# Kernel optimization log

Hardware: AMD Instinct MI355X
Metric: run time of the kernel (lower is better)

Reference implementation:

```python
import jax, jax.numpy as jnp
import numpy as np

B, S, H, OUT, L = 32, 4096, 128, 128, 3


def _log_g(x):
    return jnp.where(x >= 0, jnp.log(jax.nn.relu(x) + 0.5), -jax.nn.softplus(-x))


def _cell(x, Wz, bz, Wh, bh):
    # x: [B, S, Din] -> h: [B, S, H]
    k = x @ Wz.T + bz                              # [B,S,H]
    log_z = -jax.nn.softplus(-k)
    log_coeffs = -jax.nn.softplus(k)
    # h_0 = zeros -> log_g(0) = log(0.5)
    log_h0 = jnp.full((x.shape[0], 1, k.shape[-1]), np.log(0.5), dtype=k.dtype)
    log_tilde_h = _log_g(x @ Wh.T + bh)
    log_values = jnp.concatenate([log_h0, log_z + log_tilde_h], axis=1)  # [B,S+1,H]
    # FAITHFUL to source: cumsum over the FEATURE axis (dim=-1), pad along seq
    a_star = jnp.pad(jnp.cumsum(log_coeffs, axis=-1), ((0, 0), (1, 0), (0, 0)))
    log_h = a_star + jax.lax.cumlogsumexp(log_values - a_star, axis=1)
    # torch forward applies sigmoid to the cell output, then drops the h_0 row
    return jax.nn.sigmoid(jnp.exp(log_h))[:, 1:, :]


def setup_inputs() -> dict:
    key = jax.random.key(0)
    ks = jax.random.split(key, 2 * L + 2)
    inp = {"x": jax.random.normal(ks[0], (B, S), dtype=jnp.float32)}
    for l in range(L):
        din = 1 if l == 0 else H
        inp[f"Wz{l}"] = jax.random.normal(ks[1 + 2 * l], (H, din), dtype=jnp.float32) * 0.02
        inp[f"bz{l}"] = jnp.zeros((H,), dtype=jnp.float32)
        inp[f"Wh{l}"] = jax.random.normal(ks[2 + 2 * l], (H, din), dtype=jnp.float32) * 0.02
        inp[f"bh{l}"] = jnp.zeros((H,), dtype=jnp.float32)
    inp["Wout"] = jax.random.normal(ks[-1], (OUT, H * S), dtype=jnp.float32) * (1.0 / np.sqrt(H * S))
    inp["bout"] = jnp.zeros((OUT,), dtype=jnp.float32)
    return inp


def reference(x, Wz0, bz0, Wh0, bh0, Wz1, bz1, Wh1, bh1, Wz2, bz2, Wh2, bh2, Wout, bout):
    h = x[:, :, None]  # [B,S,1]
    for (Wz, bz, Wh, bh) in ((Wz0, bz0, Wh0, bh0), (Wz1, bz1, Wh1, bh1), (Wz2, bz2, Wh2, bh2)):
        h = _cell(h, Wz, bz, Wh, bh)
    flat = h.reshape(h.shape[0], -1)  # [B, S*H]
    return flat @ Wout.T + bout       # [B, OUT]
```

## Files before the change

### kernel.cpp

```cpp
#include <hip/hip_runtime.h>
#include <hip/hip_bf16.h>
#include <math.h>

#define B_   32
#define S_   4096
#define H_   128
#define OUT_ 128
#define P_   (B_*S_)
#define NC_  64
#define CH_  (S_/NC_)
#define NKS_ 512
#define KTOT_ (H_*S_)
#define NEGINF_ (-__builtin_inff())
#define HTP_ 136

typedef __bf16 bf16x8 __attribute__((ext_vector_type(8)));
typedef float  f32x4  __attribute__((ext_vector_type(4)));
typedef unsigned short ushort8_t __attribute__((ext_vector_type(8)));

__device__ __forceinline__ float sp_(float x) {
  return __logf(1.f + __expf(x));
}
__device__ __forceinline__ float logg_(float x) {
  float t = (x >= 0.f) ? (x + 0.5f) : __builtin_amdgcn_rcpf(1.f + __expf(-x));
  return __logf(t);
}
__device__ __forceinline__ float lae_(float a, float b) {
  float m = fmaxf(a, b);
  float d = -fabsf(a - b);
  return m + __logf(1.f + __expf(d));
}
__device__ __forceinline__ float sigm_(float e) {
  return __builtin_amdgcn_rcpf(1.f + __expf(-e));
}
__device__ __forceinline__ unsigned short f2bf_(float f) {
  unsigned int u = __float_as_uint(f);
  u += 0x7fffu + ((u >> 16) & 1u);
  return (unsigned short)(u >> 16);
}

#define DPPADD_(v, ctrl, rmask) \
  ((v) + __int_as_float(__builtin_amdgcn_update_dpp( \
      0, __float_as_int(v), (ctrl), (rmask), 0xf, true)))
__device__ __forceinline__ float wscan_(float v) {
  v = DPPADD_(v, 0x111, 0xf);
  v = DPPADD_(v, 0x112, 0xf);
  v = DPPADD_(v, 0x114, 0xf);
  v = DPPADD_(v, 0x118, 0xf);
  v = DPPADD_(v, 0x142, 0xa);
  v = DPPADD_(v, 0x143, 0xc);
  return v;
}

__global__ __launch_bounds__(256) void convw2_kernel(
    const float* __restrict__ Wz1, const float* __restrict__ Wh1,
    const float* __restrict__ Wz2, const float* __restrict__ Wh2,
    unsigned short* __restrict__ Wc1, unsigned short* __restrict__ Wc2)
{
  int idx = blockIdx.x * 256 + threadIdx.x;
  Wc1[idx] = f2bf_(idx < 16384 ? Wz1[idx] : Wh1[idx - 16384]);
  Wc2[idx] = f2bf_(idx < 16384 ? Wz2[idx] : Wh2[idx - 16384]);
}

__global__ __launch_bounds__(256) void prep0t_kernel(
    const float* __restrict__ x,
    const float* __restrict__ Wz, const float* __restrict__ bz,
    const float* __restrict__ Wh, const float* __restrict__ bh,
    float* __restrict__ u, float* __restrict__ A, float* __restrict__ tot)
{
  __shared__ float tpart[4][128];
  int lane = threadIdx.x & 63, w = threadIdx.x >> 6;
  float wz0 = Wz[lane], wz1 = Wz[lane + 64];
  float bz0 = bz[lane], bz1 = bz[lane + 64];
  float wh0 = Wh[lane], wh1 = Wh[lane + 64];
  float bh0 = bh[lane], bh1 = bh[lane + 64];
  int blk = blockIdx.x;
  size_t base = (size_t)blk * (CH_ * H_);
  int pos0 = blk * CH_;
  float t0 = NEGINF_, t1 = NEGINF_;
  for (int j = 0; j < 16; ++j) {
    int i = j * 4 + w;
    float xv = x[pos0 + i];
    float k0 = fmaf(xv, wz0, bz0), k1 = fmaf(xv, wz1, bz1);
    float g0 = fmaf(xv, wh0, bh0), g1 = fmaf(xv, wh1, bh1);
    float lc0 = -sp_(k0), lc1 = -sp_(k1);
    float lv0 = k0 + lc0 + logg_(g0);
    float lv1 = k1 + lc1 + logg_(g1);
    float s0 = wscan_(lc0);
    float c0 = __shfl(s0, 63, 64);
    float s1 = wscan_(lc1) + c0;
    float u0 = lv0 - s0, u1 = lv1 - s1;
    size_t o = base + (size_t)i * H_;
    u[o + lane]      = u0;  u[o + 64 + lane] = u1;
    A[o + lane]      = s0;  A[o + 64 + lane] = s1;
    t0 = lae_(t0, u0); t1 = lae_(t1, u1);
  }
  tpart[w][lane] = t0; tpart[w][64 + lane] = t1;
  __syncthreads();
  if (w == 0) {
    int ch = lane;
    tot[(size_t)blk * H_ + ch] =
        lae_(lae_(tpart[0][ch], tpart[1][ch]), lae_(tpart[2][ch], tpart[3][ch]));
    ch = lane + 64;
    tot[(size_t)blk * H_ + ch] =
        lae_(lae_(tpart[0][ch], tpart[1][ch]), lae_(tpart[2][ch], tpart[3][ch]));
  }
}

__global__ __launch_bounds__(128) void scan2_kernel(
    const float* __restrict__ tot, float* __restrict__ carry)
{
  int b = blockIdx.x, ch = threadIdx.x;
  float r = -0.6931471805599453f;
  for (int c = 0; c < NC_; ++c) {
    size_t idx = (size_t)(b * NC_ + c) * H_ + ch;
    carry[idx] = r;
    r = lae_(r, tot[idx]);
  }
}

__global__ __launch_bounds__(256) void kb_kernel(
    const float* __restrict__ carry,
    const unsigned short* __restrict__ Wc,
    const float* __restrict__ bz, const float* __restrict__ bh,
    float* __restrict__ u, float* __restrict__ A,
    float* __restrict__ tot)
{
  __shared__ unsigned short hT[64][HTP_];
  __shared__ float kg[16][260];
  __shared__ float scr[32][128];
  __shared__ float thand[128];
  __shared__ float tpart[4][128];
  int tid = threadIdx.x;
  int lane = tid & 63, w = tid >> 6;
  int l15 = lane & 15, quad = lane >> 4;
  int half = tid >> 7, ch = tid & 127;
  int blk = blockIdx.x;
  size_t base = (size_t)blk * (CH_ * H_);

  if (half == 0) {
    float r = carry[(size_t)blk * H_ + ch];
    const float* up = u + base + ch;
    const float* Ap = A + base + ch;
    for (int i0 = 0; i0 < 32; i0 += 16) {
      float uv[16], av[16];
      #pragma unroll
      for (int i = 0; i < 16; ++i) { uv[i] = up[(i0 + i) * H_]; av[i] = Ap[(i0 + i) * H_]; }
      #pragma unroll
      for (int i = 0; i < 16; ++i) {
        r = lae_(r, uv[i]);
        hT[i0 + i][ch] = f2bf_(sigm_(__expf(av[i] + r)));
      }
    }
    thand[ch] = r;
  } else {
    float r = NEGINF_;
    const float* up = u + base + ch;
    for (int i0 = 0; i0 < 32; i0 += 16) {
      float uv[16];
      #pragma unroll
      for (int i = 0; i < 16; ++i) uv[i] = up[(32 + i0 + i) * H_];
      #pragma unroll
      for (int i = 0; i < 16; ++i) { r = lae_(r, uv[i]); scr[i0 + i][ch] = r; }
    }
  }
  __syncthreads();
  if (half == 1) {
    float r31 = thand[ch];
    const float* Ap = A + base + ch;
    for (int i0 = 0; i0 < 32; i0 += 16) {
      float av[16];
      #pragma unroll
      for (int i = 0; i < 16; ++i) av[i] = Ap[(32 + i0 + i) * H_];
      #pragma unroll
      for (int i = 0; i < 16; ++i) {
        float ri = lae_(r31, scr[i0 + i][ch]);
        hT[32 + i0 + i][ch] = f2bf_(sigm_(__expf(av[i] + ri)));
      }
    }
  }
  __syncthreads();

  float bz0v = bz[lane], bz1v = bz[lane + 64];
  float bh0v = bh[lane], bh1v = bh[lane + 64];
  float t0 = NEGINF_, t1 = NEGINF_;

  for (int t = 0; t < 4; ++t) {
    f32x4 z = {0.f, 0.f, 0.f, 0.f};
    f32x4 acc[4] = {z, z, z, z};
    #pragma unroll
    for (int kk = 0; kk < 4; ++kk) {
      bf16x8 a = *reinterpret_cast<const bf16x8*>(&hT[t * 16 + l15][kk * 32 + quad * 8]);
      #pragma unroll
      for (int nt = 0; nt < 4; ++nt) {
        int n = w * 64 + nt * 16 + l15;
        bf16x8 bf = *reinterpret_cast<const bf16x8*>(Wc + n * 128 + kk * 32 + quad * 8);
        acc[nt] = __builtin_amdgcn_mfma_f32_16x16x32_bf16(a, bf, acc[nt], 0, 0, 0);
      }
    }
    __syncthreads();
    #pragma unroll
    for (int nt = 0; nt < 4; ++nt) {
      int col = w * 64 + nt * 16 + l15;
      #pragma unroll
      for (int r2 = 0; r2 < 4; ++r2)
        kg[quad * 4 + r2][col] = acc[nt][r2];
    }
    __syncthreads();
    #pragma unroll
    for (int i = 0; i < 4; ++i) {
      int row = w + i * 4;
      int sIdx = t * 16 + row;
      float k0 = kg[row][lane]        + bz0v;
      float k1 = kg[row][64 + lane]   + bz1v;
      float g0 = kg[row][128 + lane]  + bh0v;
      float g1 = kg[row][192 + lane]  + bh1v;
      float lc0 = -sp_(k0), lc1 = -sp_(k1);
      float lv0 = k0 + lc0 + logg_(g0);
      float lv1 = k1 + lc1 + logg_(g1);
      float s0 = wscan_(lc0);
      float c0 = __shfl(s0, 63, 64);
      float s1 = wscan_(lc1) + c0;
      float u0 = lv0 - s0, u1 = lv1 - s1;
      size_t o = base + (size_t)sIdx * H_;
      u[o + lane]      = u0;  u[o + 64 + lane] = u1;
      A[o + lane]      = s0;  A[o + 64 + lane] = s1;
      t0 = lae_(t0, u0); t1 = lae_(t1, u1);
    }
  }

  tpart[w][lane] = t0; tpart[w][64 + lane] = t1;
  __syncthreads();
  if (w == 0) {
    int c = lane;
    tot[(size_t)blk * H_ + c] =
        lae_(lae_(tpart[0][c], tpart[1][c]), lae_(tpart[2][c], tpart[3][c]));
    c = lane + 64;
    tot[(size_t)blk * H_ + c] =
        lae_(lae_(tpart[0][c], tpart[1][c]), lae_(tpart[2][c], tpart[3][c]));
  }
}

__global__ __launch_bounds__(256) void scan3v2_kernel(
    const float* __restrict__ u, const float* __restrict__ A,
    const float* __restrict__ carry, unsigned short* __restrict__ hbf)
{
  __shared__ float scr[32][128];
  __shared__ float thand[128];
  int tid = threadIdx.x;
  int half = tid >> 7, ch = tid & 127;
  int blk = blockIdx.x;
  size_t base = (size_t)blk * (CH_ * H_);
  const float* up = u + base + ch;
  const float* Ap = A + base + ch;
  unsigned short* hp = hbf + base + ch;
  if (half == 0) {
    float r = carry[(size_t)blk * H_ + ch];
    for (int i0 = 0; i0 < 32; i0 += 16) {
      float uv[16], av[16];
      #pragma unroll
      for (int i = 0; i < 16; ++i) { uv[i] = up[(i0 + i) * H_]; av[i] = Ap[(i0 + i) * H_]; }
      #pragma unroll
      for (int i = 0; i < 16; ++i) {
        r = lae_(r, uv[i]);
        hp[(size_t)(i0 + i) * H_] = f2bf_(sigm_(__expf(av[i] + r)));
      }
    }
    thand[ch] = r;
  } else {
    float r = NEGINF_;
    for (int i0 = 0; i0 < 32; i0 += 16) {
      float uv[16];
      #pragma unroll
      for (int i = 0; i < 16; ++i) uv[i] = up[(32 + i0 + i) * H_];
      #pragma unroll
      for (int i = 0; i < 16; ++i) { r = lae_(r, uv[i]); scr[i0 + i][ch] = r; }
    }
  }
  __syncthreads();
  if (half == 1) {
    float r31 = thand[ch];
    for (int i0 = 0; i0 < 32; i0 += 16) {
      float av[16];
      #pragma unroll
      for (int i = 0; i < 16; ++i) av[i] = Ap[(32 + i0 + i) * H_];
      #pragma unroll
      for (int i = 0; i < 16; ++i) {
        float ri = lae_(r31, scr[i0 + i][ch]);
        hp[(size_t)(32 + i0 + i) * H_] = f2bf_(sigm_(__expf(av[i] + ri)));
      }
    }
  }
}

__global__ __launch_bounds__(256) void outmm_kernel(
    const unsigned short* __restrict__ hbf,
    const float* __restrict__ Wout,
    float* __restrict__ part)
{
  const int KSL = KTOT_ / NKS_;
  int tid = threadIdx.x, w = tid >> 6, lane = tid & 63;
  int l15 = lane & 15, quad = lane >> 4;
  int k0base = blockIdx.x * KSL;
  f32x4 acc[2][2] = {{{0,0,0,0},{0,0,0,0}},{{0,0,0,0},{0,0,0,0}}};
  for (int ks = 0; ks < KSL; ks += 32) {
    int k0 = k0base + ks;
    bf16x8 a0 = *reinterpret_cast<const bf16x8*>(
        hbf + (size_t)l15 * KTOT_ + k0 + quad * 8);
    bf16x8 a1 = *reinterpret_cast<const bf16x8*>(
        hbf + (size_t)(16 + l15) * KTOT_ + k0 + quad * 8);
    #pragma unroll
    for (int nt = 0; nt < 2; ++nt) {
      int n = w * 32 + nt * 16 + l15;
      const float* wp = Wout + (size_t)n * KTOT_ + k0 + quad * 8;
      float4 wa = *reinterpret_cast<const float4*>(wp);
      float4 wb = *reinterpret_cast<const float4*>(wp + 4);
      ushort8_t tt;
      tt[0] = f2bf_(wa.x); tt[1] = f2bf_(wa.y); tt[2] = f2bf_(wa.z); tt[3] = f2bf_(wa.w);
      tt[4] = f2bf_(wb.x); tt[5] = f2bf_(wb.y); tt[6] = f2bf_(wb.z); tt[7] = f2bf_(wb.w);
      bf16x8 bf = __builtin_bit_cast(bf16x8, tt);
      acc[0][nt] = __builtin_amdgcn_mfma_f32_16x16x32_bf16(a0, bf, acc[0][nt], 0, 0, 0);
      acc[1][nt] = __builtin_amdgcn_mfma_f32_16x16x32_bf16(a1, bf, acc[1][nt], 0, 0, 0);
    }
  }
  float* pp = part + (size_t)blockIdx.x * (B_ * OUT_);
  #pragma unroll
  for (int mt = 0; mt < 2; ++mt)
    #pragma unroll
    for (int nt = 0; nt < 2; ++nt)
      #pragma unroll
      for (int r = 0; r < 4; ++r) {
        int b = mt * 16 + quad * 4 + r;
        int o = w * 32 + nt * 16 + l15;
        pp[b * OUT_ + o] = acc[mt][nt][r];
      }
}

__global__ __launch_bounds__(256) void outred_kernel(
    const float* __restrict__ part, const float* __restrict__ bout,
    float* __restrict__ out)
{
  int w = threadIdx.x >> 6, lane = threadIdx.x & 63;
  int idx = blockIdx.x * 4 + w;
  float s = 0.f;
  for (int wg = lane; wg < NKS_; wg += 64) s += part[(size_t)wg * (B_ * OUT_) + idx];
  #pragma unroll
  for (int d = 32; d; d >>= 1) s += __shfl_down(s, (unsigned)d, 64);
  if (lane == 0) out[idx] = s + bout[idx & (OUT_ - 1)];
}

extern "C" void kernel_launch(void* const* d_in, const int* in_sizes, int n_in,
                              void* d_out, int out_size, void* d_ws, size_t ws_size,
                              hipStream_t stream)
{
  const float* x    = (const float*)d_in[0];
  const float* Wz[3] = {(const float*)d_in[1], (const float*)d_in[5], (const float*)d_in[9]};
  const float* bz[3] = {(const float*)d_in[2], (const float*)d_in[6], (const float*)d_in[10]};
  const float* Wh[3] = {(const float*)d_in[3], (const float*)d_in[7], (const float*)d_in[11]};
  const float* bh[3] = {(const float*)d_in[4], (const float*)d_in[8], (const float*)d_in[12]};
  const float* Wout = (const float*)d_in[13];
  const float* bout = (const float*)d_in[14];
  float* out = (float*)d_out;

  char* ws = (char*)d_ws;
  float*          u     = (float*)(ws + 0);
  float*          A     = (float*)(ws + 67108864);
  unsigned short* hbf   = (unsigned short*)(ws + 134217728);
  unsigned short* Wc1   = (unsigned short*)(ws + 167772160);
  unsigned short* Wc2   = (unsigned short*)(ws + 167837696);
  float*          tot   = (float*)(ws + 167903232);
  float*          carry = (float*)(ws + 168951808);
  float*          part  = (float*)(ws + 170000384);

  convw2_kernel<<<128, 256, 0, stream>>>(Wz[1], Wh[1], Wz[2], Wh[2], Wc1, Wc2);

  prep0t_kernel<<<B_ * NC_, 256, 0, stream>>>(x, Wz[0], bz[0], Wh[0], bh[0], u, A, tot);
  scan2_kernel<<<B_, 128, 0, stream>>>(tot, carry);

  kb_kernel<<<B_ * NC_, 256, 0, stream>>>(carry, Wc1, bz[1], bh[1], u, A, tot);
  scan2_kernel<<<B_, 128, 0, stream>>>(tot, carry);
  kb_kernel<<<B_ * NC_, 256, 0, stream>>>(carry, Wc2, bz[2], bh[2], u, A, tot);
  scan2_kernel<<<B_, 128, 0, stream>>>(tot, carry);

  scan3v2_kernel<<<B_ * NC_, 256, 0, stream>>>(u, A, carry, hbf);

  outmm_kernel<<<NKS_, 256, 0, stream>>>(hbf, Wout, part);
  outred_kernel<<<(B_ * OUT_) / 4, 256, 0, stream>>>(part, bout, out);
}
```

Baseline: 667.0 us.

## Interleave u/A into float2 and fold chunk-carry scan into consumer kernels

After: 712.4 us. 6.8% more time.

```diff
diff --git a/kernel.cpp b/kernel.cpp
--- a/kernel.cpp
+++ b/kernel.cpp
@@ -12,6 +12,7 @@
 #define NKS_ 512
 #define KTOT_ (H_*S_)
 #define NEGINF_ (-__builtin_inff())
+#define LOGHALF_ (-0.6931471805599453f)
 #define HTP_ 136
 
 typedef __bf16 bf16x8 __attribute__((ext_vector_type(8)));
@@ -66,7 +67,7 @@
     const float* __restrict__ x,
     const float* __restrict__ Wz, const float* __restrict__ bz,
     const float* __restrict__ Wh, const float* __restrict__ bh,
-    float* __restrict__ u, float* __restrict__ A, float* __restrict__ tot)
+    float2* __restrict__ uA, float* __restrict__ tot)
 {
   __shared__ float tpart[4][128];
   int lane = threadIdx.x & 63, w = threadIdx.x >> 6;
@@ -91,8 +92,8 @@
     float s1 = wscan_(lc1) + c0;
     float u0 = lv0 - s0, u1 = lv1 - s1;
     size_t o = base + (size_t)i * H_;
-    u[o + lane]      = u0;  u[o + 64 + lane] = u1;
-    A[o + lane]      = s0;  A[o + 64 + lane] = s1;
+    uA[o + lane]      = make_float2(u0, s0);
+    uA[o + 64 + lane] = make_float2(u1, s1);
     t0 = lae_(t0, u0); t1 = lae_(t1, u1);
   }
   tpart[w][lane] = t0; tpart[w][64 + lane] = t1;
@@ -107,74 +108,63 @@
   }
 }
 
-__global__ __launch_bounds__(128) void scan2_kernel(
-    const float* __restrict__ tot, float* __restrict__ carry)
-{
-  int b = blockIdx.x, ch = threadIdx.x;
-  float r = -0.6931471805599453f;
-  for (int c = 0; c < NC_; ++c) {
-    size_t idx = (size_t)(b * NC_ + c) * H_ + ch;
-    carry[idx] = r;
-    r = lae_(r, tot[idx]);
-  }
-}
-
 __global__ __launch_bounds__(256) void kb_kernel(
-    const float* __restrict__ carry,
+    const float* __restrict__ totPrev,
     const unsigned short* __restrict__ Wc,
     const float* __restrict__ bz, const float* __restrict__ bh,
-    float* __restrict__ u, float* __restrict__ A,
-    float* __restrict__ tot)
+    float2* __restrict__ uA,
+    float* __restrict__ totNext)
 {
   __shared__ unsigned short hT[64][HTP_];
-  __shared__ float kg[16][260];
-  __shared__ float scr[32][128];
+  __shared__ union {
+    float kg[16][260];
+    float scr[32][128];
+  } sh;
   __shared__ float thand[128];
   __shared__ float tpart[4][128];
   int tid = threadIdx.x;
   int lane = tid & 63, w = tid >> 6;
   int l15 = lane & 15, quad = lane >> 4;
   int half = tid >> 7, ch = tid & 127;
-  int blk = blockIdx.x;
+  int blk = blockIdx.x, c = blk & (NC_ - 1);
   size_t base = (size_t)blk * (CH_ * H_);
-
-  if (half == 0) {
-    float r = carry[(size_t)blk * H_ + ch];
-    const float* up = u + base + ch;
-    const float* Ap = A + base + ch;
-    for (int i0 = 0; i0 < 32; i0 += 16) {
-      float uv[16], av[16];
-      #pragma unroll
-      for (int i = 0; i < 16; ++i) { uv[i] = up[(i0 + i) * H_]; av[i] = Ap[(i0 + i) * H_]; }
-      #pragma unroll
-      for (int i = 0; i < 16; ++i) {
-        r = lae_(r, uv[i]);
-        hT[i0 + i][ch] = f2bf_(sigm_(__expf(av[i] + r)));
+  const float2* up = uA + base + ch;
+
+  if (half == 1) {
+    float r = NEGINF_;
+    for (int i0 = 0; i0 < 32; i0 += 8) {
+      float uv[8];
+      #pragma unroll
+      for (int i = 0; i < 8; ++i) uv[i] = up[(32 + i0 + i) * H_].x;
+      #pragma unroll
+      for (int i = 0; i < 8; ++i) { r = lae_(r, uv[i]); sh.scr[i0 + i][ch] = r; }
+    }
+  } else {
+    const float* tp = totPrev + (size_t)(blk & ~(NC_ - 1)) * H_ + ch;
+    float r = LOGHALF_;
+    for (int c2 = 0; c2 < c; ++c2) r = lae_(r, tp[c2 * H_]);
+    for (int i0 = 0; i0 < 32; i0 += 8) {
+      float2 v[8];
+      #pragma unroll
+      for (int i = 0; i < 8; ++i) v[i] = up[(i0 + i) * H_];
+      #pragma unroll
+      for (int i = 0; i < 8; ++i) {
+        r = lae_(r, v[i].x);
+        hT[i0 + i][ch] = f2bf_(sigm_(__expf(v[i].y + r)));
       }
     }
     thand[ch] = r;
-  } else {
-    float r = NEGINF_;
-    const float* up = u + base + ch;
-    for (int i0 = 0; i0 < 32; i0 += 16) {
-      float uv[16];
-      #pragma unroll
-      for (int i = 0; i < 16; ++i) uv[i] = up[(32 + i0 + i) * H_];
-      #pragma unroll
-      for (int i = 0; i < 16; ++i) { r = lae_(r, uv[i]); scr[i0 + i][ch] = r; }
-    }
   }
   __syncthreads();
   if (half == 1) {
     float r31 = thand[ch];
-    const float* Ap = A + base + ch;
-    for (int i0 = 0; i0 < 32; i0 += 16) {
-      float av[16];
-      #pragma unroll
-      for (int i = 0; i < 16; ++i) av[i] = Ap[(32 + i0 + i) * H_];
-      #pragma unroll
-      for (int i = 0; i < 16; ++i) {
-        float ri = lae_(r31, scr[i0 + i][ch]);
+    for (int i0 = 0; i0 < 32; i0 += 8) {
+      float av[8];
+      #pragma unroll
+      for (int i = 0; i < 8; ++i) av[i] = up[(32 + i0 + i) * H_].y;
+      #pragma unroll
+      for (int i = 0; i < 8; ++i) {
+        float ri = lae_(r31, sh.scr[i0 + i][ch]);
         hT[32 + i0 + i][ch] = f2bf_(sigm_(__expf(av[i] + ri)));
       }
     }
@@ -204,17 +194,17 @@
       int col = w * 64 + nt * 16 + l15;
       #pragma unroll
       for (int r2 = 0; r2 < 4; ++r2)
-        kg[quad * 4 + r2][col] = acc[nt][r2];
+        sh.kg[quad * 4 + r2][col] = acc[nt][r2];
     }
     __syncthreads();
     #pragma unroll
     for (int i = 0; i < 4; ++i) {
       int row = w + i * 4;
       int sIdx = t * 16 + row;
-      float k0 = kg[row][lane]        + bz0v;
-      float k1 = kg[row][64 + lane]   + bz1v;
-      float g0 = kg[row][128 + lane]  + bh0v;
-      float g1 = kg[row][192 + lane]  + bh1v;
+      float k0 = sh.kg[row][lane]        + bz0v;
+      float k1 = sh.kg[row][64 + lane]   + bz1v;
+      float g0 = sh.kg[row][128 + lane]  + bh0v;
+      float g1 = sh.kg[row][192 + lane]  + bh1v;
       float lc0 = -sp_(k0), lc1 = -sp_(k1);
       float lv0 = k0 + lc0 + logg_(g0);
       float lv1 = k1 + lc1 + logg_(g1);
@@ -223,8 +213,8 @@
       float s1 = wscan_(lc1) + c0;
       float u0 = lv0 - s0, u1 = lv1 - s1;
       size_t o = base + (size_t)sIdx * H_;
-      u[o + lane]      = u0;  u[o + 64 + lane] = u1;
-      A[o + lane]      = s0;  A[o + 64 + lane] = s1;
+      uA[o + lane]      = make_float2(u0, s0);
+      uA[o + 64 + lane] = make_float2(u1, s1);
       t0 = lae_(t0, u0); t1 = lae_(t1, u1);
     }
   }
@@ -232,60 +222,61 @@
   tpart[w][lane] = t0; tpart[w][64 + lane] = t1;
   __syncthreads();
   if (w == 0) {
-    int c = lane;
-    tot[(size_t)blk * H_ + c] =
-        lae_(lae_(tpart[0][c], tpart[1][c]), lae_(tpart[2][c], tpart[3][c]));
-    c = lane + 64;
-    tot[(size_t)blk * H_ + c] =
-        lae_(lae_(tpart[0][c], tpart[1][c]), lae_(tpart[2][c], tpart[3][c]));
+    int cc = lane;
+    totNext[(size_t)blk * H_ + cc] =
+        lae_(lae_(tpart[0][cc], tpart[1][cc]), lae_(tpart[2][cc], tpart[3][cc]));
+    cc = lane + 64;
+    totNext[(size_t)blk * H_ + cc] =
+        lae_(lae_(tpart[0][cc], tpart[1][cc]), lae_(tpart[2][cc], tpart[3][cc]));
   }
 }
 
 __global__ __launch_bounds__(256) void scan3v2_kernel(
-    const float* __restrict__ u, const float* __restrict__ A,
-    const float* __restrict__ carry, unsigned short* __restrict__ hbf)
+    const float2* __restrict__ uA, const float* __restrict__ totPrev,
+    unsigned short* __restrict__ hbf)
 {
   __shared__ float scr[32][128];
   __shared__ float thand[128];
   int tid = threadIdx.x;
   int half = tid >> 7, ch = tid & 127;
-  int blk = blockIdx.x;
+  int blk = blockIdx.x, c = blk & (NC_ - 1);
   size_t base = (size_t)blk * (CH_ * H_);
-  const float* up = u + base + ch;
-  const float* Ap = A + base + ch;
+  const float2* up = uA + base + ch;
   unsigned short* hp = hbf + base + ch;
-  if (half == 0) {
-    float r = carry[(size_t)blk * H_ + ch];
-    for (int i0 = 0; i0 < 32; i0 += 16) {
-      float uv[16], av[16];
-      #pragma unroll
-      for (int i = 0; i < 16; ++i) { uv[i] = up[(i0 + i) * H_]; av[i] = Ap[(i0 + i) * H_]; }
-      #pragma unroll
-      for (int i = 0; i < 16; ++i) {
-        r = lae_(r, uv[i]);
-        hp[(size_t)(i0 + i) * H_] = f2bf_(sigm_(__expf(av[i] + r)));
+  if (half == 1) {
+    float r = NEGINF_;
+    for (int i0 = 0; i0 < 32; i0 += 8) {
+      float uv[8];
+      #pragma unroll
+      for (int i = 0; i < 8; ++i) uv[i] = up[(32 + i0 + i) * H_].x;
+      #pragma unroll
+      for (int i = 0; i < 8; ++i) { r = lae_(r, uv[i]); scr[i0 + i][ch] = r; }
+    }
+  } else {
+    const float* tp = totPrev + (size_t)(blk & ~(NC_ - 1)) * H_ + ch;
+    float r = LOGHALF_;
+    for (int c2 = 0; c2 < c; ++c2) r = lae_(r, tp[c2 * H_]);
+    for (int i0 = 0; i0 < 32; i0 += 8) {
+      float2 v[8];
+      #pragma unroll
+      for (int i = 0; i < 8; ++i) v[i] = up[(i0 + i) * H_];
+      #pragma unroll
+      for (int i = 0; i < 8; ++i) {
+        r = lae_(r, v[i].x);
+        hp[(size_t)(i0 + i) * H_] = f2bf_(sigm_(__expf(v[i].y + r)));
       }
     }
     thand[ch] = r;
-  } else {
-    float r = NEGINF_;
-    for (int i0 = 0; i0 < 32; i0 += 16) {
-      float uv[16];
-      #pragma unroll
-      for (int i = 0; i < 16; ++i) uv[i] = up[(32 + i0 + i) * H_];
-      #pragma unroll
-      for (int i = 0; i < 16; ++i) { r = lae_(r, uv[i]); scr[i0 + i][ch] = r; }
-    }
   }
   __syncthreads();
   if (half == 1) {
     float r31 = thand[ch];
-    for (int i0 = 0; i0 < 32; i0 += 16) {
-      float av[16];
-      #pragma unroll
-      for (int i = 0; i < 16; ++i) av[i] = Ap[(32 + i0 + i) * H_];
-      #pragma unroll
-      for (int i = 0; i < 16; ++i) {
+    for (int i0 = 0; i0 < 32; i0 += 8) {
+      float av[8];
+      #pragma unroll
+      for (int i = 0; i < 8; ++i) av[i] = up[(32 + i0 + i) * H_].y;
+      #pragma unroll
+      for (int i = 0; i < 8; ++i) {
         float ri = lae_(r31, scr[i0 + i][ch]);
         hp[(size_t)(32 + i0 + i) * H_] = f2bf_(sigm_(__expf(av[i] + ri)));
       }
@@ -363,26 +354,23 @@
   float* out = (float*)d_out;
 
   char* ws = (char*)d_ws;
-  float*          u     = (float*)(ws + 0);
-  float*          A     = (float*)(ws + 67108864);
+  float2*         uA    = (float2*)(ws + 0);
   unsigned short* hbf   = (unsigned short*)(ws + 134217728);
   unsigned short* Wc1   = (unsigned short*)(ws + 167772160);
   unsigned short* Wc2   = (unsigned short*)(ws + 167837696);
-  float*          tot   = (float*)(ws + 167903232);
-  float*          carry = (float*)(ws + 168951808);
-  float*          part  = (float*)(ws + 170000384);
+  float*          tot0  = (float*)(ws + 167903232);
+  float*          tot1  = (float*)(ws + 168951808);
+  float*          tot2  = (float*)(ws + 170000384);
+  float*          part  = (float*)(ws + 0);
 
   convw2_kernel<<<128, 256, 0, stream>>>(Wz[1], Wh[1], Wz[2], Wh[2], Wc1, Wc2);
 
-  prep0t_kernel<<<B_ * NC_, 256, 0, stream>>>(x, Wz[0], bz[0], Wh[0], bh[0], u, A, tot);
-  scan2_kernel<<<B_, 128, 0, stream>>>(tot, carry);
-
-  kb_kernel<<<B_ * NC_, 256, 0, stream>>>(carry, Wc1, bz[1], bh[1], u, A, tot);
-  scan2_kernel<<<B_, 128, 0, stream>>>(tot, carry);
-  kb_kernel<<<B_ * NC_, 256, 0, stream>>>(carry, Wc2, bz[2], bh[2], u, A, tot);
-  scan2_kernel<<<B_, 128, 0, stream>>>(tot, carry);
-
-  scan3v2_kernel<<<B_ * NC_, 256, 0, stream>>>(u, A, carry, hbf);
+  prep0t_kernel<<<B_ * NC_, 256, 0, stream>>>(x, Wz[0], bz[0], Wh[0], bh[0], uA, tot0);
+
+  kb_kernel<<<B_ * NC_, 256, 0, stream>>>(tot0, Wc1, bz[1], bh[1], uA, tot1);
+  kb_kernel<<<B_ * NC_, 256, 0, stream>>>(tot1, Wc2, bz[2], bh[2], uA, tot2);
+
+  scan3v2_kernel<<<B_ * NC_, 256, 0, stream>>>(uA, tot2, hbf);
 
   outmm_kernel<<<NKS_, 256, 0, stream>>>(hbf, Wout, part);
   outred_kernel<<<(B_ * OUT_) / 4, 256, 0, stream>>>(part, bout, out);
```
